# Kernel tuning notes

Measured on AMD Instinct MI355X. Metric: run time of the kernel, lower is better.

## Reference

```python
import jax, jax.numpy as jnp
import numpy as np

N, DZ, L, H, MLPH, INC = 256, 256, 256, 512, 2048, 8
CAT_IDX = np.arange(0, 192, 2)                      # 96 categorical token positions (interleaved)
NUM_IDX = np.setdiff1d(np.arange(L), CAT_IDX)       # 160 numerical token positions
CARDS = [4, 16, 128]                                # cardinality per categorical group
GSZ = 32                                            # tokens per categorical group
NUM_CARD = 100                                      # cardinality of quantized numerical params


def setup_inputs() -> dict:
    ks = list(jax.random.split(jax.random.key(0), 24))
    def nrm(shape, s=0.02):
        return jax.random.normal(ks.pop(), shape, jnp.float32) * s
    inp = {}
    inp['z'] = jax.random.normal(ks.pop(), (N, DZ), jnp.float32)
    inp['mlp_w0'] = nrm((DZ, MLPH)); inp['mlp_b0'] = jnp.zeros((MLPH,), jnp.float32)
    inp['mlp_w1'] = nrm((MLPH, MLPH)); inp['mlp_b1'] = jnp.zeros((MLPH,), jnp.float32)
    inp['mlp_w2'] = nrm((MLPH, MLPH)); inp['mlp_b2'] = jnp.zeros((MLPH,), jnp.float32)
    inp['conv_w'] = nrm((H, INC)); inp['conv_b'] = jnp.zeros((H,), jnp.float32)
    for g, card in enumerate(CARDS):
        inp[f'cat_w{g}'] = nrm((H, card)); inp[f'cat_b{g}'] = jnp.zeros((card,), jnp.float32)
    inp['num_w'] = nrm((H, 2)); inp['num_b'] = jnp.zeros((2,), jnp.float32)
    inp['num_target'] = jax.random.uniform(ks.pop(), (N, len(NUM_IDX)), jnp.float32)
    inp['cat_target'] = jax.random.randint(ks.pop(), (N, len(CAT_IDX)), 0, 4, jnp.int32)
    return inp


def reference(z, mlp_w0, mlp_b0, mlp_w1, mlp_b1, mlp_w2, mlp_b2, conv_w, conv_b,
              cat_w0, cat_b0, cat_w1, cat_b1, cat_w2, cat_b2, num_w, num_b,
              num_target, cat_target):
    n = z.shape[0]
    # MLP: fc0 -> act -> fc1 -> act -> fc2
    h = z @ mlp_w0 + mlp_b0
    h = jax.nn.relu(h) @ mlp_w1 + mlp_b1
    h = jax.nn.relu(h) @ mlp_w2 + mlp_b2
    h = h.reshape(n, INC, L)                        # (N, C=8, L)
    # act + 1x1 conv to hidden_size, then transpose -> (N, L, H)
    u = jnp.einsum('ncl,hc->nlh', jax.nn.relu(h), conv_w) + conv_b
    # ---- categorical tokens: gather, per-cardinality heads, CE NLL, argmax sample ----
    hc = u[:, CAT_IDX, :]                           # (N, 96, H)
    heads = [(cat_w0, cat_b0), (cat_w1, cat_b1), (cat_w2, cat_b2)]
    nlls, samps = [], []
    for g, (w, b) in enumerate(heads):
        hg = hc[:, g * GSZ:(g + 1) * GSZ, :]        # (N, 32, H)
        logits = hg @ w + b                         # (N, 32, card)
        logp = jax.nn.log_softmax(logits, axis=-1)
        tg = cat_target[:, g * GSZ:(g + 1) * GSZ]
        nlls.append(-jnp.take_along_axis(logp, tg[..., None], axis=-1)[..., 0])
        samps.append(jnp.argmax(logits, axis=-1))
    cat_nll = jnp.concatenate(nlls, axis=1)         # (N, 96)
    cat_samples = jnp.concatenate(samps, axis=1)    # (N, 96)
    # ---- numerical tokens: gather, 2-param discretized logistic, NLL, mode sample ----
    hn = u[:, NUM_IDX, :]                           # (N, 160, H)
    p = hn @ num_w + num_b                          # (N, 160, 2)
    mu = jax.nn.sigmoid(p[..., 0])
    s = jax.nn.softplus(p[..., 1]) + 1e-4
    hb = 1.0 / (2.0 * (NUM_CARD - 1))               # half bin width
    t = num_target
    cdf_p = jax.nn.sigmoid((t + hb - mu) / s)
    cdf_m = jax.nn.sigmoid((t - hb - mu) / s)
    prob = jnp.where(t < hb, cdf_p, jnp.where(t > 1.0 - hb, 1.0 - cdf_m, cdf_p - cdf_m))
    num_nll = -jnp.log(jnp.maximum(prob, 1e-7))     # (N, 160)
    num_samples = jax.lax.stop_gradient(jnp.round(mu * (NUM_CARD - 1)) / (NUM_CARD - 1))
    # ---- scatter samples back into the preallocated output tensor ----
    u_out = jnp.zeros((n, L, 3), jnp.float32)
    u_out = u_out.at[:, CAT_IDX, 0].set(cat_samples.astype(jnp.float32))
    u_out = u_out.at[:, NUM_IDX, 1].set(num_samples)
    return u_out, cat_nll, num_nll
```

## Files before the change

kernel.cpp:

```cpp
#include <hip/hip_runtime.h>
#include <hip/hip_fp16.h>
#include <math.h>

#define NN   256
#define LL   256
#define HH   512
#define MLPHv 2048
#define INCv 8
#define NCOLS 150

typedef _Float16 f16x8 __attribute__((ext_vector_type(8)));
typedef float    f32x4 __attribute__((ext_vector_type(4)));

__device__ __forceinline__ void pack8(const float* fv, uint4& hv, uint4& lv)
{
    unsigned short h[8], l[8];
#pragma unroll
    for (int j = 0; j < 8; ++j) {
        __half hh = __float2half_rn(fv[j]);
        h[j] = __half_as_ushort(hh);
        float rem = fv[j] - __half2float(hh);
        l[j] = __half_as_ushort(__float2half_rn(rem * 4096.f));
    }
    hv.x = (unsigned)h[0] | ((unsigned)h[1] << 16);
    hv.y = (unsigned)h[2] | ((unsigned)h[3] << 16);
    hv.z = (unsigned)h[4] | ((unsigned)h[5] << 16);
    hv.w = (unsigned)h[6] | ((unsigned)h[7] << 16);
    lv.x = (unsigned)l[0] | ((unsigned)l[1] << 16);
    lv.y = (unsigned)l[2] | ((unsigned)l[3] << 16);
    lv.z = (unsigned)l[4] | ((unsigned)l[5] << 16);
    lv.w = (unsigned)l[6] | ((unsigned)l[7] << 16);
}

template <bool DIRECT>
__global__ __launch_bounds__(512, 2) void gemmhl(
    const float* __restrict__ A, const float* __restrict__ W,
    const float* __restrict__ bias, float* __restrict__ outp,
    int K, int kchunk, int nsteps)
{
    __shared__ unsigned short sAh[8192];
    __shared__ unsigned short sAl[8192];
    __shared__ unsigned short sBh[8192];
    __shared__ unsigned short sBl[8192];

    const int tid   = threadIdx.x;
    const int bn    = blockIdx.x * 128;
    const int bm    = blockIdx.y * 128;
    const int kbase = blockIdx.z * kchunk;
    const int lane  = tid & 63;
    const int wv    = tid >> 6, wr = wv >> 2, wc = wv & 3;
    const int rA    = tid >> 2, ktA = (tid & 3) << 4;
    const int nW    = tid & 127, kqW = tid >> 7;

    f32x4 accH[4][2], accC[4][2];
#pragma unroll
    for (int r = 0; r < 4; ++r)
#pragma unroll
        for (int c = 0; c < 2; ++c) {
            accH[r][c] = (f32x4){0.f, 0.f, 0.f, 0.f};
            accC[r][c] = (f32x4){0.f, 0.f, 0.f, 0.f};
        }

    float aReg[16], wReg[16];

    {
        const float* pA = &A[(size_t)(bm + rA) * K + kbase + ktA];
#pragma unroll
        for (int q = 0; q < 4; ++q) {
            float4 v = *(const float4*)(pA + q * 4);
            aReg[q * 4 + 0] = v.x; aReg[q * 4 + 1] = v.y;
            aReg[q * 4 + 2] = v.z; aReg[q * 4 + 3] = v.w;
        }
#pragma unroll
        for (int j = 0; j < 16; ++j)
            wReg[j] = W[(size_t)(kbase + kqW * 16 + j) * 2048 + bn + nW];
    }

    for (int t = 0; t < nsteps; ++t) {
#pragma unroll
        for (int o2 = 0; o2 < 2; ++o2) {
            uint4 hv, lv;
            pack8(&aReg[o2 * 8], hv, lv);
            const int oo   = ((tid & 3) << 1) + o2;
            const int base = ((oo >> 2) << 12) + ((rA >> 4) << 9)
                           + (((rA & 15) + ((oo & 3) << 4)) << 3);
            *(uint4*)&sAh[base] = hv;
            *(uint4*)&sAl[base] = lv;
        }
#pragma unroll
        for (int o2 = 0; o2 < 2; ++o2) {
            uint4 hv, lv;
            pack8(&wReg[o2 * 8], hv, lv);
            const int oo   = (kqW << 1) + o2;
            const int base = ((oo >> 2) << 12) + ((nW >> 4) << 9)
                           + (((nW & 15) + ((oo & 3) << 4)) << 3);
            *(uint4*)&sBh[base] = hv;
            *(uint4*)&sBl[base] = lv;
        }

        if (t + 1 < nsteps) {
            const int kb = kbase + (t + 1) * 64;
            const float* pA = &A[(size_t)(bm + rA) * K + kb + ktA];
#pragma unroll
            for (int q = 0; q < 4; ++q) {
                float4 v = *(const float4*)(pA + q * 4);
                aReg[q * 4 + 0] = v.x; aReg[q * 4 + 1] = v.y;
                aReg[q * 4 + 2] = v.z; aReg[q * 4 + 3] = v.w;
            }
#pragma unroll
            for (int j = 0; j < 16; ++j)
                wReg[j] = W[(size_t)(kb + kqW * 16 + j) * 2048 + bn + nW];
        }

        __syncthreads();

#pragma unroll
        for (int s = 0; s < 2; ++s) {
            f16x8 aH[4], aL[4], bH[2], bL[2];
#pragma unroll
            for (int r = 0; r < 4; ++r) {
                const int off = (s << 12) + (((wr << 2) + r) << 9) + (lane << 3);
                aH[r] = *(const f16x8*)&sAh[off];
                aL[r] = *(const f16x8*)&sAl[off];
            }
#pragma unroll
            for (int c = 0; c < 2; ++c) {
                const int off = (s << 12) + (((wc << 1) + c) << 9) + (lane << 3);
                bH[c] = *(const f16x8*)&sBh[off];
                bL[c] = *(const f16x8*)&sBl[off];
            }
#pragma unroll
            for (int r = 0; r < 4; ++r)
#pragma unroll
                for (int c = 0; c < 2; ++c) {
                    accH[r][c] = __builtin_amdgcn_mfma_f32_16x16x32_f16(aH[r], bH[c], accH[r][c], 0, 0, 0);
                    accC[r][c] = __builtin_amdgcn_mfma_f32_16x16x32_f16(aH[r], bL[c], accC[r][c], 0, 0, 0);
                    accC[r][c] = __builtin_amdgcn_mfma_f32_16x16x32_f16(aL[r], bH[c], accC[r][c], 0, 0, 0);
                }
        }
        __syncthreads();
    }

    const float inv = 1.f / 4096.f;
    float* pout = DIRECT ? outp : (outp + (size_t)blockIdx.z * 524288);
#pragma unroll
    for (int r = 0; r < 4; ++r)
#pragma unroll
        for (int c = 0; c < 2; ++c) {
            const int row = bm + wr * 64 + r * 16 + ((lane >> 4) << 2);
            const int col = bn + wc * 32 + c * 16 + (lane & 15);
            const float vb = DIRECT ? bias[col] : 0.f;
#pragma unroll
            for (int e = 0; e < 4; ++e) {
                float v = accH[r][c][e] + accC[r][c][e] * inv;
                if (DIRECT) v = fmaxf(v + vb, 0.f);
                pout[(size_t)(row + e) * 2048 + col] = v;
            }
        }
}

__global__ __launch_bounds__(256) void reduce_bias_relu(
    const float* __restrict__ part, const float* __restrict__ bias,
    float* __restrict__ out, int ksplit)
{
    const int r  = blockIdx.x;
    const int ct = r & 15, rg = r >> 4;
    const int e  = threadIdx.x * 4;
    const int row = rg * 8 + (e >> 7);
    const int col = ct * 128 + (e & 127);
    const size_t idx = (size_t)row * 2048 + col;
    float4 s = *(const float4*)&bias[col];
    for (int k = 0; k < ksplit; ++k) {
        const float4 p = *(const float4*)&part[(size_t)k * 524288 + idx];
        s.x += p.x; s.y += p.y; s.z += p.z; s.w += p.w;
    }
    s.x = fmaxf(s.x, 0.f); s.y = fmaxf(s.y, 0.f);
    s.z = fmaxf(s.z, 0.f); s.w = fmaxf(s.w, 0.f);
    *(float4*)&out[idx] = s;
}

__global__ __launch_bounds__(256) void fuse_heads_kernel(
    const float* __restrict__ conv_w, const float* __restrict__ conv_b,
    const float* __restrict__ cw0, const float* __restrict__ cb0,
    const float* __restrict__ cw1, const float* __restrict__ cb1,
    const float* __restrict__ cw2, const float* __restrict__ cb2,
    const float* __restrict__ nw,  const float* __restrict__ nb,
    float* __restrict__ Mf, float* __restrict__ beta)
{
    int k = blockIdx.x;
    const float* W; const float* B; int off, card;
    if (k < 4)        { W = cw0; B = cb0; off = 0;   card = 4;   }
    else if (k < 20)  { W = cw1; B = cb1; off = 4;   card = 16;  }
    else if (k < 148) { W = cw2; B = cb2; off = 20;  card = 128; }
    else              { W = nw;  B = nb;  off = 148; card = 2;   }
    int kc  = k - off;
    int tid = threadIdx.x;
    float part[INCv + 1];
#pragma unroll
    for (int c = 0; c <= INCv; ++c) part[c] = 0.f;
    for (int h = tid; h < HH; h += 256) {
        float wv = W[h * card + kc];
#pragma unroll
        for (int c = 0; c < INCv; ++c) part[c] += conv_w[h * INCv + c] * wv;
        part[INCv] += conv_b[h] * wv;
    }
    __shared__ float red[256];
    for (int c = 0; c <= INCv; ++c) {
        red[tid] = part[c];
        __syncthreads();
        for (int s2 = 128; s2 > 0; s2 >>= 1) {
            if (tid < s2) red[tid] += red[tid + s2];
            __syncthreads();
        }
        if (tid == 0) {
            if (c < INCv) Mf[c * NCOLS + k] = red[0];
            else          beta[k] = red[0] + B[kc];
        }
        __syncthreads();
    }
}

__global__ __launch_bounds__(256) void cat_kernel(
    const float* __restrict__ rh, const float* __restrict__ Mf,
    const float* __restrict__ beta, const int* __restrict__ cat_target,
    float* __restrict__ out)
{
    const int g = blockIdx.y;
    const int card = (g == 0) ? 4 : (g == 1) ? 16 : 128;
    const int off  = (g == 0) ? 0 : (g == 1) ? 4  : 20;
    __shared__ float Ms[INCv][128];
    __shared__ float Bsh[128];
    const int tid = threadIdx.x;
    for (int i = tid; i < card * INCv; i += 256) {
        int c = i / card, k = i % card;
        Ms[c][k] = Mf[c * NCOLS + off + k];
    }
    for (int i = tid; i < card; i += 256) Bsh[i] = beta[off + i];
    __syncthreads();

    const int idx = blockIdx.x * 256 + tid;
    const int n = idx >> 5, j = idx & 31;
    const int ci = g * 32 + j;
    const int l  = ci * 2;
    float rv[INCv];
#pragma unroll
    for (int c = 0; c < INCv; ++c) rv[c] = rh[n * MLPHv + c * LL + l];

    float mx = -1e30f; int arg = 0;
    for (int k = 0; k < card; ++k) {
        float s = Bsh[k];
#pragma unroll
        for (int c = 0; c < INCv; ++c) s += rv[c] * Ms[c][k];
        if (s > mx) { mx = s; arg = k; }
    }
    const int tg = cat_target[n * 96 + ci];
    float sum = 0.f, stg = 0.f;
    for (int k = 0; k < card; ++k) {
        float s = Bsh[k];
#pragma unroll
        for (int c = 0; c < INCv; ++c) s += rv[c] * Ms[c][k];
        sum += expf(s - mx);
        if (k == tg) stg = s;
    }
    float lse = mx + logf(sum);
    out[NN * LL * 3 + n * 96 + ci] = lse - stg;
    float* u = out + (size_t)(n * LL + l) * 3;
    u[0] = (float)arg; u[1] = 0.f; u[2] = 0.f;
}

__global__ __launch_bounds__(256) void num_kernel(
    const float* __restrict__ rh, const float* __restrict__ Mf,
    const float* __restrict__ beta, const float* __restrict__ num_target,
    float* __restrict__ out)
{
    const int idx = blockIdx.x * 256 + threadIdx.x;
    const int n = idx / 160, ni = idx % 160;
    const int l = (ni < 96) ? (2 * ni + 1) : (96 + ni);
    float rv[INCv];
#pragma unroll
    for (int c = 0; c < INCv; ++c) rv[c] = rh[n * MLPHv + c * LL + l];
    float p0 = beta[148], p1 = beta[149];
#pragma unroll
    for (int c = 0; c < INCv; ++c) {
        p0 += rv[c] * Mf[c * NCOLS + 148];
        p1 += rv[c] * Mf[c * NCOLS + 149];
    }
    float mu = 1.f / (1.f + expf(-p0));
    float sp = (p1 > 20.f) ? p1 : log1pf(expf(p1));
    float s  = sp + 1e-4f;
    const float hb = 1.f / 198.f;
    float t  = num_target[n * 160 + ni];
    float cp = 1.f / (1.f + expf(-((t + hb - mu) / s)));
    float cm = 1.f / (1.f + expf(-((t - hb - mu) / s)));
    float prob = (t < hb) ? cp : ((t > 1.f - hb) ? (1.f - cm) : (cp - cm));
    out[NN * LL * 3 + NN * 96 + n * 160 + ni] = -logf(fmaxf(prob, 1e-7f));
    float* u = out + (size_t)(n * LL + l) * 3;
    u[0] = 0.f; u[1] = rintf(mu * 99.f) / 99.f; u[2] = 0.f;
}

extern "C" void kernel_launch(void* const* d_in, const int* in_sizes, int n_in,
                              void* d_out, int out_size, void* d_ws, size_t ws_size,
                              hipStream_t stream)
{
    const float* z   = (const float*)d_in[0];
    const float* w0  = (const float*)d_in[1];
    const float* b0  = (const float*)d_in[2];
    const float* w1  = (const float*)d_in[3];
    const float* b1  = (const float*)d_in[4];
    const float* w2  = (const float*)d_in[5];
    const float* b2  = (const float*)d_in[6];
    const float* cvw = (const float*)d_in[7];
    const float* cvb = (const float*)d_in[8];
    const float* cw0 = (const float*)d_in[9];
    const float* cb0 = (const float*)d_in[10];
    const float* cw1 = (const float*)d_in[11];
    const float* cb1 = (const float*)d_in[12];
    const float* cw2 = (const float*)d_in[13];
    const float* cb2 = (const float*)d_in[14];
    const float* nw  = (const float*)d_in[15];
    const float* nb  = (const float*)d_in[16];
    const float* num_target = (const float*)d_in[17];
    const int*   cat_target = (const int*)d_in[18];
    float* out = (float*)d_out;
    float* ws  = (float*)d_ws;

    float* rh0  = ws;
    float* rh1  = ws + 524288;
    float* rh2  = ws + 1048576;
    float* Mf   = ws + 1572864;
    float* beta = Mf + 8 * NCOLS;
    const size_t PART_OFF = 1575936;
    float* part = ws + PART_OFF;
    const size_t avail_f = ws_size / sizeof(float);
    int ksplit = 0;
    if      (PART_OFF + 8ull * 524288 <= avail_f) ksplit = 8;
    else if (PART_OFF + 4ull * 524288 <= avail_f) ksplit = 4;
    else if (PART_OFF + 2ull * 524288 <= avail_f) ksplit = 2;
    else if (PART_OFF + 1ull * 524288 <= avail_f) ksplit = 1;

    fuse_heads_kernel<<<dim3(NCOLS), 256, 0, stream>>>(
        cvw, cvb, cw0, cb0, cw1, cb1, cw2, cb2, nw, nb, Mf, beta);

    if (ksplit > 0) {
        const int ks0 = (ksplit > 4) ? 4 : ksplit;
        const int kc0 = 256 / ks0;
        gemmhl<false><<<dim3(16, 2, ks0), 512, 0, stream>>>(z, w0, nullptr, part, 256, kc0, kc0 / 64);
        reduce_bias_relu<<<dim3(512), 256, 0, stream>>>(part, b0, rh0, ks0);

        const int kc = 2048 / ksplit;
        gemmhl<false><<<dim3(16, 2, ksplit), 512, 0, stream>>>(rh0, w1, nullptr, part, 2048, kc, kc / 64);
        reduce_bias_relu<<<dim3(512), 256, 0, stream>>>(part, b1, rh1, ksplit);

        gemmhl<false><<<dim3(16, 2, ksplit), 512, 0, stream>>>(rh1, w2, nullptr, part, 2048, kc, kc / 64);
        reduce_bias_relu<<<dim3(512), 256, 0, stream>>>(part, b2, rh2, ksplit);
    } else {
        gemmhl<true><<<dim3(16, 2, 1), 512, 0, stream>>>(z,   w0, b0, rh0, 256,  256,  4);
        gemmhl<true><<<dim3(16, 2, 1), 512, 0, stream>>>(rh0, w1, b1, rh1, 2048, 2048, 32);
        gemmhl<true><<<dim3(16, 2, 1), 512, 0, stream>>>(rh1, w2, b2, rh2, 2048, 2048, 32);
    }

    cat_kernel<<<dim3(32, 3), 256, 0, stream>>>(rh2, Mf, beta, cat_target, out);
    num_kernel<<<dim3(160),   256, 0, stream>>>(rh2, Mf, beta, num_target, out);
}
```

Before: 83.58 us.

## Pre-split activations into fp16 hi/lo and merge small kernels

Activations are now split into fp16 high/low pairs once, either in a prep kernel for z or in the epilogues that produce them. The GEMM therefore loads ready-made halves and no longer converts A on every tile. The first GEMM drops split-K and applies bias+ReLU directly, the head-fusion and z-split work are merged into one prep kernel, and the cat and num kernels become a single launch. The change cuts launch count, conversion ALU work and A-side bytes. In exchange it drops the workspace-size fallback and hardcodes ksplit=8, which assumes a large enough workspace.

```diff
diff --git a/kernel.cpp b/kernel.cpp
--- a/kernel.cpp
+++ b/kernel.cpp
@@ -11,17 +11,20 @@
 
 typedef _Float16 f16x8 __attribute__((ext_vector_type(8)));
 typedef float    f32x4 __attribute__((ext_vector_type(4)));
+typedef unsigned short ushort_t;
+
+__device__ __forceinline__ void split1(float f, ushort_t& h, ushort_t& l)
+{
+    __half hh = __float2half_rn(f);
+    h = __half_as_ushort(hh);
+    l = __half_as_ushort(__float2half_rn((f - __half2float(hh)) * 4096.f));
+}
 
 __device__ __forceinline__ void pack8(const float* fv, uint4& hv, uint4& lv)
 {
-    unsigned short h[8], l[8];
-#pragma unroll
-    for (int j = 0; j < 8; ++j) {
-        __half hh = __float2half_rn(fv[j]);
-        h[j] = __half_as_ushort(hh);
-        float rem = fv[j] - __half2float(hh);
-        l[j] = __half_as_ushort(__float2half_rn(rem * 4096.f));
-    }
+    ushort_t h[8], l[8];
+#pragma unroll
+    for (int j = 0; j < 8; ++j) split1(fv[j], h[j], l[j]);
     hv.x = (unsigned)h[0] | ((unsigned)h[1] << 16);
     hv.y = (unsigned)h[2] | ((unsigned)h[3] << 16);
     hv.z = (unsigned)h[4] | ((unsigned)h[5] << 16);
@@ -32,16 +35,77 @@
     lv.w = (unsigned)l[6] | ((unsigned)l[7] << 16);
 }
 
-template <bool DIRECT>
+__global__ __launch_bounds__(256) void prep_kernel(
+    const float* __restrict__ z,
+    const float* __restrict__ conv_w, const float* __restrict__ conv_b,
+    const float* __restrict__ cw0, const float* __restrict__ cb0,
+    const float* __restrict__ cw1, const float* __restrict__ cb1,
+    const float* __restrict__ cw2, const float* __restrict__ cb2,
+    const float* __restrict__ nw,  const float* __restrict__ nb,
+    float* __restrict__ Mf, float* __restrict__ beta,
+    ushort_t* __restrict__ zh, ushort_t* __restrict__ zl)
+{
+    const int bx  = blockIdx.x;
+    const int tid = threadIdx.x;
+    if (bx >= 150) {
+        const int base = (bx - 150) * 2048 + tid * 8;
+        float fv[8];
+        float4 v0 = *(const float4*)&z[base];
+        float4 v1 = *(const float4*)&z[base + 4];
+        fv[0]=v0.x; fv[1]=v0.y; fv[2]=v0.z; fv[3]=v0.w;
+        fv[4]=v1.x; fv[5]=v1.y; fv[6]=v1.z; fv[7]=v1.w;
+        uint4 hv, lv;
+        pack8(fv, hv, lv);
+        *(uint4*)&zh[base] = hv;
+        *(uint4*)&zl[base] = lv;
+        return;
+    }
+    const int k = bx;
+    const float* W; const float* B; int off, card;
+    if (k < 4)        { W = cw0; B = cb0; off = 0;   card = 4;   }
+    else if (k < 20)  { W = cw1; B = cb1; off = 4;   card = 16;  }
+    else if (k < 148) { W = cw2; B = cb2; off = 20;  card = 128; }
+    else              { W = nw;  B = nb;  off = 148; card = 2;   }
+    const int kc = k - off;
+    float part[INCv + 1];
+#pragma unroll
+    for (int c = 0; c <= INCv; ++c) part[c] = 0.f;
+#pragma unroll
+    for (int it = 0; it < 2; ++it) {
+        const int h = tid + it * 256;
+        const float wv = W[h * card + kc];
+#pragma unroll
+        for (int c = 0; c < INCv; ++c) part[c] += conv_w[h * INCv + c] * wv;
+        part[INCv] += conv_b[h] * wv;
+    }
+    __shared__ float red[INCv + 1][4];
+    const int lane = tid & 63, wave = tid >> 6;
+#pragma unroll
+    for (int c = 0; c <= INCv; ++c) {
+        float v = part[c];
+#pragma unroll
+        for (int o = 32; o >= 1; o >>= 1) v += __shfl_down(v, o, 64);
+        if (lane == 0) red[c][wave] = v;
+    }
+    __syncthreads();
+    if (tid <= INCv) {
+        const float s = red[tid][0] + red[tid][1] + red[tid][2] + red[tid][3];
+        if (tid < INCv) Mf[tid * NCOLS + k] = s;
+        else            beta[k] = s + B[kc];
+    }
+}
+
+template <int OUTMODE>
 __global__ __launch_bounds__(512, 2) void gemmhl(
-    const float* __restrict__ A, const float* __restrict__ W,
-    const float* __restrict__ bias, float* __restrict__ outp,
+    const ushort_t* __restrict__ Ah, const ushort_t* __restrict__ Al,
+    const float* __restrict__ W, const float* __restrict__ bias,
+    float* __restrict__ outp, ushort_t* __restrict__ outH, ushort_t* __restrict__ outL,
     int K, int kchunk, int nsteps)
 {
-    __shared__ unsigned short sAh[8192];
-    __shared__ unsigned short sAl[8192];
-    __shared__ unsigned short sBh[8192];
-    __shared__ unsigned short sBl[8192];
+    __shared__ ushort_t sAh[8192];
+    __shared__ ushort_t sAl[8192];
+    __shared__ ushort_t sBh[8192];
+    __shared__ ushort_t sBl[8192];
 
     const int tid   = threadIdx.x;
     const int bn    = blockIdx.x * 128;
@@ -61,16 +125,14 @@
             accC[r][c] = (f32x4){0.f, 0.f, 0.f, 0.f};
         }
 
-    float aReg[16], wReg[16];
+    uint4 aRegH[2], aRegL[2];
+    float wReg[16];
 
     {
-        const float* pA = &A[(size_t)(bm + rA) * K + kbase + ktA];
-#pragma unroll
-        for (int q = 0; q < 4; ++q) {
-            float4 v = *(const float4*)(pA + q * 4);
-            aReg[q * 4 + 0] = v.x; aReg[q * 4 + 1] = v.y;
-            aReg[q * 4 + 2] = v.z; aReg[q * 4 + 3] = v.w;
-        }
+        const ushort_t* pH = Ah + (size_t)(bm + rA) * K + kbase + ktA;
+        const ushort_t* pL = Al + (size_t)(bm + rA) * K + kbase + ktA;
+        aRegH[0] = *(const uint4*)pH; aRegH[1] = *(const uint4*)(pH + 8);
+        aRegL[0] = *(const uint4*)pL; aRegL[1] = *(const uint4*)(pL + 8);
 #pragma unroll
         for (int j = 0; j < 16; ++j)
             wReg[j] = W[(size_t)(kbase + kqW * 16 + j) * 2048 + bn + nW];
@@ -79,13 +141,11 @@
     for (int t = 0; t < nsteps; ++t) {
 #pragma unroll
         for (int o2 = 0; o2 < 2; ++o2) {
-            uint4 hv, lv;
-            pack8(&aReg[o2 * 8], hv, lv);
             const int oo   = ((tid & 3) << 1) + o2;
             const int base = ((oo >> 2) << 12) + ((rA >> 4) << 9)
                            + (((rA & 15) + ((oo & 3) << 4)) << 3);
-            *(uint4*)&sAh[base] = hv;
-            *(uint4*)&sAl[base] = lv;
+            *(uint4*)&sAh[base] = aRegH[o2];
+            *(uint4*)&sAl[base] = aRegL[o2];
         }
 #pragma unroll
         for (int o2 = 0; o2 < 2; ++o2) {
@@ -100,13 +160,10 @@
 
         if (t + 1 < nsteps) {
             const int kb = kbase + (t + 1) * 64;
-            const float* pA = &A[(size_t)(bm + rA) * K + kb + ktA];
-#pragma unroll
-            for (int q = 0; q < 4; ++q) {
-                float4 v = *(const float4*)(pA + q * 4);
-                aReg[q * 4 + 0] = v.x; aReg[q * 4 + 1] = v.y;
-                aReg[q * 4 + 2] = v.z; aReg[q * 4 + 3] = v.w;
-            }
+            const ushort_t* pH = Ah + (size_t)(bm + rA) * K + kb + ktA;
+            const ushort_t* pL = Al + (size_t)(bm + rA) * K + kb + ktA;
+            aRegH[0] = *(const uint4*)pH; aRegH[1] = *(const uint4*)(pH + 8);
+            aRegL[0] = *(const uint4*)pL; aRegL[1] = *(const uint4*)(pL + 8);
 #pragma unroll
             for (int j = 0; j < 16; ++j)
                 wReg[j] = W[(size_t)(kb + kqW * 16 + j) * 2048 + bn + nW];
@@ -142,26 +199,32 @@
     }
 
     const float inv = 1.f / 4096.f;
-    float* pout = DIRECT ? outp : (outp + (size_t)blockIdx.z * 524288);
 #pragma unroll
     for (int r = 0; r < 4; ++r)
 #pragma unroll
         for (int c = 0; c < 2; ++c) {
             const int row = bm + wr * 64 + r * 16 + ((lane >> 4) << 2);
             const int col = bn + wc * 32 + c * 16 + (lane & 15);
-            const float vb = DIRECT ? bias[col] : 0.f;
 #pragma unroll
             for (int e = 0; e < 4; ++e) {
                 float v = accH[r][c][e] + accC[r][c][e] * inv;
-                if (DIRECT) v = fmaxf(v + vb, 0.f);
-                pout[(size_t)(row + e) * 2048 + col] = v;
+                if (OUTMODE == 1) {
+                    v = fmaxf(v + bias[col], 0.f);
+                    ushort_t h, l;
+                    split1(v, h, l);
+                    outH[(size_t)(row + e) * 2048 + col] = h;
+                    outL[(size_t)(row + e) * 2048 + col] = l;
+                } else {
+                    (outp + (size_t)blockIdx.z * 524288)[(size_t)(row + e) * 2048 + col] = v;
+                }
             }
         }
 }
 
-__global__ __launch_bounds__(256) void reduce_bias_relu(
+template <bool SPLITOUT>
+__global__ __launch_bounds__(256) void reduce_k(
     const float* __restrict__ part, const float* __restrict__ bias,
-    float* __restrict__ out, int ksplit)
+    float* __restrict__ outF, ushort_t* __restrict__ outH, ushort_t* __restrict__ outL)
 {
     const int r  = blockIdx.x;
     const int ct = r & 15, rg = r >> 4;
@@ -170,132 +233,99 @@
     const int col = ct * 128 + (e & 127);
     const size_t idx = (size_t)row * 2048 + col;
     float4 s = *(const float4*)&bias[col];
-    for (int k = 0; k < ksplit; ++k) {
+#pragma unroll
+    for (int k = 0; k < 8; ++k) {
         const float4 p = *(const float4*)&part[(size_t)k * 524288 + idx];
         s.x += p.x; s.y += p.y; s.z += p.z; s.w += p.w;
     }
     s.x = fmaxf(s.x, 0.f); s.y = fmaxf(s.y, 0.f);
     s.z = fmaxf(s.z, 0.f); s.w = fmaxf(s.w, 0.f);
-    *(float4*)&out[idx] = s;
-}
-
-__global__ __launch_bounds__(256) void fuse_heads_kernel(
-    const float* __restrict__ conv_w, const float* __restrict__ conv_b,
-    const float* __restrict__ cw0, const float* __restrict__ cb0,
-    const float* __restrict__ cw1, const float* __restrict__ cb1,
-    const float* __restrict__ cw2, const float* __restrict__ cb2,
-    const float* __restrict__ nw,  const float* __restrict__ nb,
-    float* __restrict__ Mf, float* __restrict__ beta)
-{
-    int k = blockIdx.x;
-    const float* W; const float* B; int off, card;
-    if (k < 4)        { W = cw0; B = cb0; off = 0;   card = 4;   }
-    else if (k < 20)  { W = cw1; B = cb1; off = 4;   card = 16;  }
-    else if (k < 148) { W = cw2; B = cb2; off = 20;  card = 128; }
-    else              { W = nw;  B = nb;  off = 148; card = 2;   }
-    int kc  = k - off;
-    int tid = threadIdx.x;
-    float part[INCv + 1];
-#pragma unroll
-    for (int c = 0; c <= INCv; ++c) part[c] = 0.f;
-    for (int h = tid; h < HH; h += 256) {
-        float wv = W[h * card + kc];
-#pragma unroll
-        for (int c = 0; c < INCv; ++c) part[c] += conv_w[h * INCv + c] * wv;
-        part[INCv] += conv_b[h] * wv;
-    }
-    __shared__ float red[256];
-    for (int c = 0; c <= INCv; ++c) {
-        red[tid] = part[c];
-        __syncthreads();
-        for (int s2 = 128; s2 > 0; s2 >>= 1) {
-            if (tid < s2) red[tid] += red[tid + s2];
-            __syncthreads();
-        }
-        if (tid == 0) {
-            if (c < INCv) Mf[c * NCOLS + k] = red[0];
-            else          beta[k] = red[0] + B[kc];
-        }
-        __syncthreads();
-    }
-}
-
-__global__ __launch_bounds__(256) void cat_kernel(
+    if (SPLITOUT) {
+        ushort_t h[4], l[4];
+        split1(s.x, h[0], l[0]); split1(s.y, h[1], l[1]);
+        split1(s.z, h[2], l[2]); split1(s.w, h[3], l[3]);
+        ushort4 hv = {h[0], h[1], h[2], h[3]};
+        ushort4 lv = {l[0], l[1], l[2], l[3]};
+        *(ushort4*)&outH[idx] = hv;
+        *(ushort4*)&outL[idx] = lv;
+    } else {
+        *(float4*)&outF[idx] = s;
+    }
+}
+
+__global__ __launch_bounds__(256) void heads_kernel(
     const float* __restrict__ rh, const float* __restrict__ Mf,
     const float* __restrict__ beta, const int* __restrict__ cat_target,
-    float* __restrict__ out)
-{
-    const int g = blockIdx.y;
-    const int card = (g == 0) ? 4 : (g == 1) ? 16 : 128;
-    const int off  = (g == 0) ? 0 : (g == 1) ? 4  : 20;
+    const float* __restrict__ num_target, float* __restrict__ out)
+{
+    const int bx  = blockIdx.x;
+    const int tid = threadIdx.x;
     __shared__ float Ms[INCv][128];
     __shared__ float Bsh[128];
-    const int tid = threadIdx.x;
-    for (int i = tid; i < card * INCv; i += 256) {
-        int c = i / card, k = i % card;
-        Ms[c][k] = Mf[c * NCOLS + off + k];
-    }
-    for (int i = tid; i < card; i += 256) Bsh[i] = beta[off + i];
-    __syncthreads();
-
-    const int idx = blockIdx.x * 256 + tid;
-    const int n = idx >> 5, j = idx & 31;
-    const int ci = g * 32 + j;
-    const int l  = ci * 2;
-    float rv[INCv];
-#pragma unroll
-    for (int c = 0; c < INCv; ++c) rv[c] = rh[n * MLPHv + c * LL + l];
-
-    float mx = -1e30f; int arg = 0;
-    for (int k = 0; k < card; ++k) {
-        float s = Bsh[k];
-#pragma unroll
-        for (int c = 0; c < INCv; ++c) s += rv[c] * Ms[c][k];
-        if (s > mx) { mx = s; arg = k; }
-    }
-    const int tg = cat_target[n * 96 + ci];
-    float sum = 0.f, stg = 0.f;
-    for (int k = 0; k < card; ++k) {
-        float s = Bsh[k];
-#pragma unroll
-        for (int c = 0; c < INCv; ++c) s += rv[c] * Ms[c][k];
-        sum += expf(s - mx);
-        if (k == tg) stg = s;
-    }
-    float lse = mx + logf(sum);
-    out[NN * LL * 3 + n * 96 + ci] = lse - stg;
-    float* u = out + (size_t)(n * LL + l) * 3;
-    u[0] = (float)arg; u[1] = 0.f; u[2] = 0.f;
-}
-
-__global__ __launch_bounds__(256) void num_kernel(
-    const float* __restrict__ rh, const float* __restrict__ Mf,
-    const float* __restrict__ beta, const float* __restrict__ num_target,
-    float* __restrict__ out)
-{
-    const int idx = blockIdx.x * 256 + threadIdx.x;
-    const int n = idx / 160, ni = idx % 160;
-    const int l = (ni < 96) ? (2 * ni + 1) : (96 + ni);
-    float rv[INCv];
-#pragma unroll
-    for (int c = 0; c < INCv; ++c) rv[c] = rh[n * MLPHv + c * LL + l];
-    float p0 = beta[148], p1 = beta[149];
-#pragma unroll
-    for (int c = 0; c < INCv; ++c) {
-        p0 += rv[c] * Mf[c * NCOLS + 148];
-        p1 += rv[c] * Mf[c * NCOLS + 149];
-    }
-    float mu = 1.f / (1.f + expf(-p0));
-    float sp = (p1 > 20.f) ? p1 : log1pf(expf(p1));
-    float s  = sp + 1e-4f;
-    const float hb = 1.f / 198.f;
-    float t  = num_target[n * 160 + ni];
-    float cp = 1.f / (1.f + expf(-((t + hb - mu) / s)));
-    float cm = 1.f / (1.f + expf(-((t - hb - mu) / s)));
-    float prob = (t < hb) ? cp : ((t > 1.f - hb) ? (1.f - cm) : (cp - cm));
-    out[NN * LL * 3 + NN * 96 + n * 160 + ni] = -logf(fmaxf(prob, 1e-7f));
-    float* u = out + (size_t)(n * LL + l) * 3;
-    u[0] = 0.f; u[1] = rintf(mu * 99.f) / 99.f; u[2] = 0.f;
+    if (bx < 96) {
+        const int g = bx >> 5;
+        const int card = (g == 0) ? 4 : (g == 1) ? 16 : 128;
+        const int off  = (g == 0) ? 0 : (g == 1) ? 4  : 20;
+        for (int i = tid; i < card * INCv; i += 256) {
+            int c = i / card, k = i % card;
+            Ms[c][k] = Mf[c * NCOLS + off + k];
+        }
+        for (int i = tid; i < card; i += 256) Bsh[i] = beta[off + i];
+        __syncthreads();
+
+        const int idx = (bx & 31) * 256 + tid;
+        const int n = idx >> 5, j = idx & 31;
+        const int ci = g * 32 + j;
+        const int l  = ci * 2;
+        float rv[INCv];
+#pragma unroll
+        for (int c = 0; c < INCv; ++c) rv[c] = rh[n * MLPHv + c * LL + l];
+
+        float mx = -1e30f; int arg = 0;
+        for (int k = 0; k < card; ++k) {
+            float s = Bsh[k];
+#pragma unroll
+            for (int c = 0; c < INCv; ++c) s += rv[c] * Ms[c][k];
+            if (s > mx) { mx = s; arg = k; }
+        }
+        const int tg = cat_target[n * 96 + ci];
+        float sum = 0.f, stg = 0.f;
+        for (int k = 0; k < card; ++k) {
+            float s = Bsh[k];
+#pragma unroll
+            for (int c = 0; c < INCv; ++c) s += rv[c] * Ms[c][k];
+            sum += expf(s - mx);
+            if (k == tg) stg = s;
+        }
+        float lse = mx + logf(sum);
+        out[NN * LL * 3 + n * 96 + ci] = lse - stg;
+        float* u = out + (size_t)(n * LL + l) * 3;
+        u[0] = (float)arg; u[1] = 0.f; u[2] = 0.f;
+    } else {
+        const int idx = (bx - 96) * 256 + tid;
+        const int n = idx / 160, ni = idx % 160;
+        const int l = (ni < 96) ? (2 * ni + 1) : (96 + ni);
+        float rv[INCv];
+#pragma unroll
+        for (int c = 0; c < INCv; ++c) rv[c] = rh[n * MLPHv + c * LL + l];
+        float p0 = beta[148], p1 = beta[149];
+#pragma unroll
+        for (int c = 0; c < INCv; ++c) {
+            p0 += rv[c] * Mf[c * NCOLS + 148];
+            p1 += rv[c] * Mf[c * NCOLS + 149];
+        }
+        float mu = 1.f / (1.f + expf(-p0));
+        float sp = (p1 > 20.f) ? p1 : log1pf(expf(p1));
+        float s  = sp + 1e-4f;
+        const float hb = 1.f / 198.f;
+        float t  = num_target[n * 160 + ni];
+        float cp = 1.f / (1.f + expf(-((t + hb - mu) / s)));
+        float cm = 1.f / (1.f + expf(-((t - hb - mu) / s)));
+        float prob = (t < hb) ? cp : ((t > 1.f - hb) ? (1.f - cm) : (cp - cm));
+        out[NN * LL * 3 + NN * 96 + n * 160 + ni] = -logf(fmaxf(prob, 1e-7f));
+        float* u = out + (size_t)(n * LL + l) * 3;
+        u[0] = 0.f; u[1] = rintf(mu * 99.f) / 99.f; u[2] = 0.f;
+    }
 }
 
 extern "C" void kernel_launch(void* const* d_in, const int* in_sizes, int n_in,
@@ -324,41 +354,32 @@
     float* out = (float*)d_out;
     float* ws  = (float*)d_ws;
 
-    float* rh0  = ws;
-    float* rh1  = ws + 524288;
-    float* rh2  = ws + 1048576;
-    float* Mf   = ws + 1572864;
-    float* beta = Mf + 8 * NCOLS;
-    const size_t PART_OFF = 1575936;
-    float* part = ws + PART_OFF;
-    const size_t avail_f = ws_size / sizeof(float);
-    int ksplit = 0;
-    if      (PART_OFF + 8ull * 524288 <= avail_f) ksplit = 8;
-    else if (PART_OFF + 4ull * 524288 <= avail_f) ksplit = 4;
-    else if (PART_OFF + 2ull * 524288 <= avail_f) ksplit = 2;
-    else if (PART_OFF + 1ull * 524288 <= avail_f) ksplit = 1;
-
-    fuse_heads_kernel<<<dim3(NCOLS), 256, 0, stream>>>(
-        cvw, cvb, cw0, cb0, cw1, cb1, cw2, cb2, nw, nb, Mf, beta);
-
-    if (ksplit > 0) {
-        const int ks0 = (ksplit > 4) ? 4 : ksplit;
-        const int kc0 = 256 / ks0;
-        gemmhl<false><<<dim3(16, 2, ks0), 512, 0, stream>>>(z, w0, nullptr, part, 256, kc0, kc0 / 64);
-        reduce_bias_relu<<<dim3(512), 256, 0, stream>>>(part, b0, rh0, ks0);
-
-        const int kc = 2048 / ksplit;
-        gemmhl<false><<<dim3(16, 2, ksplit), 512, 0, stream>>>(rh0, w1, nullptr, part, 2048, kc, kc / 64);
-        reduce_bias_relu<<<dim3(512), 256, 0, stream>>>(part, b1, rh1, ksplit);
-
-        gemmhl<false><<<dim3(16, 2, ksplit), 512, 0, stream>>>(rh1, w2, nullptr, part, 2048, kc, kc / 64);
-        reduce_bias_relu<<<dim3(512), 256, 0, stream>>>(part, b2, rh2, ksplit);
-    } else {
-        gemmhl<true><<<dim3(16, 2, 1), 512, 0, stream>>>(z,   w0, b0, rh0, 256,  256,  4);
-        gemmhl<true><<<dim3(16, 2, 1), 512, 0, stream>>>(rh0, w1, b1, rh1, 2048, 2048, 32);
-        gemmhl<true><<<dim3(16, 2, 1), 512, 0, stream>>>(rh1, w2, b2, rh2, 2048, 2048, 32);
-    }
-
-    cat_kernel<<<dim3(32, 3), 256, 0, stream>>>(rh2, Mf, beta, cat_target, out);
-    num_kernel<<<dim3(160),   256, 0, stream>>>(rh2, Mf, beta, num_target, out);
-}
+    size_t o = 0;
+    float*    part = ws;                       o += 8ull * 524288;
+    float*    rh2  = ws + o;                   o += 524288;
+    float*    Mf   = ws + o;                   o += 1536;
+    float*    beta = ws + o;                   o += 256;
+    ushort_t* zh   = (ushort_t*)(ws + o);      o += 32768;
+    ushort_t* zl   = (ushort_t*)(ws + o);      o += 32768;
+    ushort_t* r0h  = (ushort_t*)(ws + o);      o += 262144;
+    ushort_t* r0l  = (ushort_t*)(ws + o);      o += 262144;
+    ushort_t* r1h  = (ushort_t*)(ws + o);      o += 262144;
+    ushort_t* r1l  = (ushort_t*)(ws + o);      o += 262144;
+
+    prep_kernel<<<dim3(182), 256, 0, stream>>>(
+        z, cvw, cvb, cw0, cb0, cw1, cb1, cw2, cb2, nw, nb, Mf, beta, zh, zl);
+
+    gemmhl<1><<<dim3(16, 2, 1), 512, 0, stream>>>(
+        zh, zl, w0, b0, nullptr, r0h, r0l, 256, 256, 4);
+
+    gemmhl<0><<<dim3(16, 2, 8), 512, 0, stream>>>(
+        r0h, r0l, w1, nullptr, part, nullptr, nullptr, 2048, 256, 4);
+    reduce_k<true><<<dim3(512), 256, 0, stream>>>(part, b1, nullptr, r1h, r1l);
+
+    gemmhl<0><<<dim3(16, 2, 8), 512, 0, stream>>>(
+        r1h, r1l, w2, nullptr, part, nullptr, nullptr, 2048, 256, 4);
+    reduce_k<false><<<dim3(512), 256, 0, stream>>>(part, b2, rh2, nullptr, nullptr);
+
+    heads_kernel<<<dim3(256), 256, 0, stream>>>(
+        rh2, Mf, beta, cat_target, num_target, out);
+}
```

Measured after the change: 140.4 us. +68.0%, slower.
